# Kernel optimization log

Hardware: AMD Instinct MI355X
Metric: run time of the kernel (lower is better)

The kernel has to match this reference:

```python
import jax, jax.numpy as jnp
import numpy as np

NUM_CLASSES = 151  # Visual Genome object classes
PRED_DIM = 51      # predicate distribution channels (50 predicates + bg)


def _conv2d(x, w, pad):
    # x: [B, Cin, H, W], w: [Cout, Cin, kh, kw]
    return jax.lax.conv_general_dilated(
        x, w, window_strides=(1, 1), padding=[(pad, pad), (pad, pad)],
        dimension_numbers=("NCHW", "OIHW", "NCHW"))


def setup_inputs() -> dict:
    key = jax.random.key(0)
    ks = jax.random.split(key, 12)
    B, N, D = 64, 80, 4096
    K = D // 4  # 1024
    s = 0.02
    return {
        "encoder_reps": jax.random.normal(ks[0], (B, N, D), jnp.float32),
        "obj_preds": jax.random.randint(ks[1], (B, N), 0, NUM_CLASSES, jnp.int32),
        "freq_table": jax.random.normal(ks[2], (NUM_CLASSES * NUM_CLASSES, PRED_DIM), jnp.float32),
        "W_comp": jax.random.normal(ks[3], (D, K), jnp.float32) * s,
        "W_ou1": jax.random.normal(ks[4], (K, K), jnp.float32) * s,
        "W_ofc": jax.random.normal(ks[5], (K, K), jnp.float32) * s,
        "W_decomp": jax.random.normal(ks[6], (K, D), jnp.float32) * s,
        "conv1": jax.random.normal(ks[7], (10, PRED_DIM, 3, 3), jnp.float32) * s,
        "conv2": jax.random.normal(ks[8], (5, 10, 3, 3), jnp.float32) * s,
        "conv3": jax.random.normal(ks[9], (1, 5, 1, 1), jnp.float32) * s,
    }


def reference(encoder_reps, obj_preds, freq_table, W_comp, W_ou1, W_ofc,
              W_decomp, conv1, conv2, conv3):
    B, N, D = encoder_reps.shape
    # obj_comp: Linear(D, D//4, bias=False) + ReLU
    comp = jax.nn.relu(jnp.einsum("bnd,dk->bnk", encoder_reps, W_comp))  # [B,N,K]
    # ou1: Linear(K, K, bias=False) + ReLU
    obj_u1 = jax.nn.relu(jnp.einsum("bnk,kj->bnj", comp, W_ou1))          # [B,N,K]
    # pairwise product indices -> freq_bias.index_with_labels (subj*C + obj)
    pair_idx = obj_preds[:, :, None] * NUM_CLASSES + obj_preds[:, None, :]  # [B,N,N]
    rel_u1 = freq_table[pair_idx]                                          # [B,N,N,51]
    # adjacency via small conv stack + sigmoid
    x = jnp.transpose(rel_u1, (0, 3, 1, 2))      # [B,51,N,N]
    x = _conv2d(x, conv1, pad=1)                 # [B,10,N,N]
    x = _conv2d(x, conv2, pad=1)                 # [B,5,N,N]
    x = _conv2d(x, conv3, pad=0)                 # [B,1,N,N]
    adj = jax.nn.sigmoid(x[:, 0])                # [B,N,N]
    # normalized Laplacian: D^-1/2 (A + I) D^-1/2
    A_hat = adj + jnp.eye(N, dtype=adj.dtype)[None]
    d = (jnp.sum(A_hat, axis=2) + 1e-5) ** (-0.5)                          # [B,N]
    L_hat = d[:, :, None] * A_hat * d[:, None, :]                          # [B,N,N]
    ofl_u = jnp.einsum("bnm,bmk->bnk", L_hat, obj_u1)                      # [B,N,K]
    # ofc_u + obj_decomp + residual
    u_m = jax.nn.relu(jnp.einsum("bnk,kj->bnj", ofl_u, W_ofc))
    decomp = jax.nn.relu(jnp.einsum("bnk,kd->bnd", u_m, W_decomp))
    return decomp + encoder_reps
```

## Files before the change

kernel.cpp:

```cpp
#include <hip/hip_runtime.h>
#include <hip/hip_bf16.h>
#include <math.h>

typedef __bf16 bf16x8 __attribute__((ext_vector_type(8)));
typedef float floatx4 __attribute__((ext_vector_type(4)));
typedef float float4v __attribute__((ext_vector_type(4)));
typedef float float2v __attribute__((ext_vector_type(2)));
typedef unsigned short ushortx4 __attribute__((ext_vector_type(4)));
typedef unsigned short ushortx8 __attribute__((ext_vector_type(8)));

__device__ __forceinline__ unsigned short f2bf(float f) {
    unsigned int u = __builtin_bit_cast(unsigned int, f);
    u += 0x7FFFu + ((u >> 16) & 1u);
    return (unsigned short)(u >> 16);
}
__device__ __forceinline__ float bf2f(unsigned short h) {
    unsigned int u = ((unsigned int)h) << 16;
    return __builtin_bit_cast(float, u);
}

__device__ __forceinline__ void gload_lds16(const void* g, void* l) {
    __builtin_amdgcn_global_load_lds(
        (const __attribute__((address_space(1))) unsigned int*)g,
        (__attribute__((address_space(3))) unsigned int*)l, 16, 0, 0);
}

__global__ __launch_bounds__(256) void cast_bf16_kernel(
    const float* __restrict__ in, unsigned short* __restrict__ out, long n8)
{
    long i = (long)blockIdx.x * 256 + threadIdx.x;
    long stride = (long)gridDim.x * 256;
    for (; i < n8; i += stride) {
        float4v a = reinterpret_cast<const float4v*>(in)[2 * i];
        float4v b = reinterpret_cast<const float4v*>(in)[2 * i + 1];
        ushortx8 h;
        #pragma unroll
        for (int q = 0; q < 4; ++q) { h[q] = f2bf(a[q]); h[4 + q] = f2bf(b[q]); }
        reinterpret_cast<ushortx8*>(out)[i] = h;
    }
}

__global__ __launch_bounds__(256) void reduce_relu_kernel(
    const unsigned short* __restrict__ p, unsigned short* __restrict__ out,
    long n8, long half_elems)
{
    long i = (long)blockIdx.x * 256 + threadIdx.x;
    long stride = (long)gridDim.x * 256;
    const ushortx8* p0 = reinterpret_cast<const ushortx8*>(p);
    const ushortx8* p1 = reinterpret_cast<const ushortx8*>(p + half_elems);
    for (; i < n8; i += stride) {
        ushortx8 a = p0[i], b = p1[i];
        ushortx8 h;
        #pragma unroll
        for (int q = 0; q < 8; ++q)
            h[q] = f2bf(fmaxf(bf2f(a[q]) + bf2f(b[q]), 0.0f));
        reinterpret_cast<ushortx8*>(out)[i] = h;
    }
}

__global__ __launch_bounds__(256) void prep_kernel(
    const float* __restrict__ w1, const float* __restrict__ w2,
    const float* __restrict__ w3, float* __restrict__ W1e,
    float* __restrict__ w23)
{
    for (int idx = threadIdx.x; idx < 4590; idx += 256) {
        int ci = idx / 90, rem = idx % 90;
        int tap = rem / 10, co = rem % 10;
        int di = tap / 3, dj = tap % 3;
        W1e[idx] = w1[((co * 51 + ci) * 3 + di) * 3 + dj];
    }
    if (threadIdx.x < 90) {
        int tap = threadIdx.x / 10, c10 = threadIdx.x % 10;
        int di = tap / 3, dj = tap % 3;
        float s = 0.f;
        #pragma unroll
        for (int c5 = 0; c5 < 5; ++c5)
            s = fmaf(w3[c5], w2[((c5 * 10 + c10) * 3 + di) * 3 + dj], s);
        w23[threadIdx.x] = s;
    }
}

__global__ __launch_bounds__(256) void fp1_kernel(
    const float* __restrict__ freq, const float* __restrict__ W1e,
    float* __restrict__ Fp1)
{
    __shared__ float W1s[4590];
    for (int idx = threadIdx.x; idx < 4590; idx += 256)
        W1s[idx] = W1e[idx];
    __syncthreads();
    int p = blockIdx.x * 256 + threadIdx.x;
    if (p >= 22801) return;
    float2v acc[45];
    #pragma unroll
    for (int t = 0; t < 45; ++t) { acc[t][0] = 0.f; acc[t][1] = 0.f; }
    const float* fr = freq + (size_t)p * 51;
    for (int ci = 0; ci < 51; ++ci) {
        float v = fr[ci];
        const float2v* wrow = reinterpret_cast<const float2v*>(&W1s[ci * 90]);
        #pragma unroll
        for (int t = 0; t < 45; ++t) {
            float2v w = wrow[t];
            acc[t][0] = fmaf(v, w[0], acc[t][0]);
            acc[t][1] = fmaf(v, w[1], acc[t][1]);
        }
    }
    float2v* out = reinterpret_cast<float2v*>(Fp1 + (size_t)p * 90);
    #pragma unroll
    for (int t = 0; t < 45; ++t) out[t] = acc[t];
}

__global__ __launch_bounds__(320) void gather_kernel(
    const int* __restrict__ preds, const float* __restrict__ Fp1,
    float* __restrict__ h1)
{
    __shared__ int pb[80];
    const int b = blockIdx.y;
    const int tid = threadIdx.x;
    if (tid < 80) pb[tid] = preds[b * 80 + tid];
    __syncthreads();
    const int i = blockIdx.x * 4 + tid / 80;
    const int j = tid % 80;
    float2v acc[5];
    #pragma unroll
    for (int q = 0; q < 5; ++q) { acc[q][0] = 0.f; acc[q][1] = 0.f; }
    #pragma unroll
    for (int di = 0; di < 3; ++di) {
        int ii = i + di - 1;
        if (ii < 0 || ii >= 80) continue;
        int pi = pb[ii] * 151;
        #pragma unroll
        for (int dj = 0; dj < 3; ++dj) {
            int jj = j + dj - 1;
            if (jj < 0 || jj >= 80) continue;
            const float2v* row = reinterpret_cast<const float2v*>(
                Fp1 + (size_t)(pi + pb[jj]) * 90 + (di * 3 + dj) * 10);
            #pragma unroll
            for (int q = 0; q < 5; ++q) {
                float2v v = row[q];
                acc[q][0] += v[0];
                acc[q][1] += v[1];
            }
        }
    }
    float2v* out = reinterpret_cast<float2v*>(
        h1 + ((size_t)b * 6400 + i * 80 + j) * 10);
    #pragma unroll
    for (int q = 0; q < 5; ++q) out[q] = acc[q];
}

__global__ __launch_bounds__(320) void conv23_kernel(
    const float* __restrict__ h1, const float* __restrict__ w23g,
    float* __restrict__ adj)
{
    __shared__ float w23s[90];
    const int tid = threadIdx.x;
    if (tid < 90) w23s[tid] = w23g[tid];
    __syncthreads();
    const int b = blockIdx.y;
    const int i = blockIdx.x * 4 + tid / 80;
    const int j = tid % 80;
    float t = 0.f;
    #pragma unroll
    for (int di = 0; di < 3; ++di) {
        int ii = i + di - 1;
        if (ii < 0 || ii >= 80) continue;
        #pragma unroll
        for (int dj = 0; dj < 3; ++dj) {
            int jj = j + dj - 1;
            if (jj < 0 || jj >= 80) continue;
            const float2v* hp = reinterpret_cast<const float2v*>(
                h1 + ((size_t)b * 6400 + ii * 80 + jj) * 10);
            const float* wp = w23s + (di * 3 + dj) * 10;
            #pragma unroll
            for (int q = 0; q < 5; ++q) {
                float2v v = hp[q];
                t = fmaf(v[0], wp[2 * q], t);
                t = fmaf(v[1], wp[2 * q + 1], t);
            }
        }
    }
    adj[(size_t)b * 6400 + i * 80 + j] = 1.0f / (1.0f + __expf(-t));
}

__global__ __launch_bounds__(128) void degree_kernel(
    const float* __restrict__ adj, float* __restrict__ deg)
{
    int b = blockIdx.x;
    int i = threadIdx.x;
    if (i >= 80) return;
    const float* row = adj + (size_t)b * 6400 + i * 80;
    float s = 1.0f + 1e-5f;
    for (int jj = 0; jj < 80; ++jj) s += row[jj];
    deg[b * 80 + i] = rsqrtf(s);
}

__global__ __launch_bounds__(256) void transpose_cast(
    const float* __restrict__ in, unsigned short* __restrict__ out,
    int R, int C)
{
    __shared__ float t[32][33];
    const int tx = threadIdx.x & 31;
    const int ty = threadIdx.x >> 5;
    const int r0 = blockIdx.y * 32, c0 = blockIdx.x * 32;
    #pragma unroll
    for (int k = 0; k < 4; ++k)
        t[ty + k * 8][tx] = in[(size_t)(r0 + ty + k * 8) * C + c0 + tx];
    __syncthreads();
    #pragma unroll
    for (int k = 0; k < 4; ++k)
        out[(size_t)(c0 + ty + k * 8) * R + r0 + tx] = f2bf(t[tx][ty + k * 8]);
}

template<int MODE>
__global__ __launch_bounds__(256) void gemm_pipe(
    const unsigned short* __restrict__ Ap, const unsigned short* __restrict__ Bt,
    void* __restrict__ Cp, const float* __restrict__ Rp,
    int M, int N, int lda, int kh)
{
    __shared__ unsigned short Al[3][128 * 32];
    __shared__ unsigned short Bl[3][128 * 32];

    const int tid  = threadIdx.x;
    const int bm   = blockIdx.x * 128;
    const int bn   = blockIdx.y * 128;
    const int zoff = blockIdx.z * kh;
    const int wave = tid >> 6;
    const int lane = tid & 63;
    const int wm   = (wave >> 1) * 64;
    const int wn   = (wave & 1) * 64;
    const int lr   = lane & 15;
    const int lk   = (lane >> 4) * 8;
    const int lkz  = lk ^ ((lr & 1) << 3) ^ (((lr >> 1) & 1) << 4);

    floatx4 acc[4][4];
    #pragma unroll
    for (int i = 0; i < 4; ++i)
        #pragma unroll
        for (int j = 0; j < 4; ++j)
            #pragma unroll
            for (int r = 0; r < 4; ++r) acc[i][j][r] = 0.0f;

    auto stage = [&](int buf, int k0) {
        #pragma unroll
        for (int it = 0; it < 2; ++it) {
            int idx = tid + it * 256;
            int r = idx >> 2, kc = (idx & 3) * 8;
            int kcz = kc ^ ((r & 1) << 3) ^ (((r >> 1) & 1) << 4);
            gload_lds16(&Ap[(size_t)(bm + r) * lda + k0 + kcz],
                        &Al[buf][idx * 8]);
        }
        #pragma unroll
        for (int it = 0; it < 2; ++it) {
            int idx = tid + it * 256;
            int r = idx >> 2, kc = (idx & 3) * 8;
            int kcz = kc ^ ((r & 1) << 3) ^ (((r >> 1) & 1) << 4);
            gload_lds16(&Bt[(size_t)(bn + r) * lda + k0 + kcz],
                        &Bl[buf][idx * 8]);
        }
    };

    const int nt = kh >> 5;
    stage(0, zoff);
    if (nt > 1) stage(1, zoff + 32);

    for (int t = 0; t < nt; ++t) {
        if (t < nt - 1) {
            asm volatile("s_waitcnt vmcnt(4)" ::: "memory");
        } else {
            asm volatile("s_waitcnt vmcnt(0)" ::: "memory");
        }
        __builtin_amdgcn_s_barrier();
        __builtin_amdgcn_sched_barrier(0);
        if (t + 2 < nt) stage((t + 2) % 3, zoff + ((t + 2) << 5));

        const int cur = t % 3;
        bf16x8 af[4], bfv[4];
        #pragma unroll
        for (int mi = 0; mi < 4; ++mi)
            af[mi] = *reinterpret_cast<const bf16x8*>(
                &Al[cur][(wm + mi * 16 + lr) * 32 + lkz]);
        #pragma unroll
        for (int ni = 0; ni < 4; ++ni)
            bfv[ni] = *reinterpret_cast<const bf16x8*>(
                &Bl[cur][(wn + ni * 16 + lr) * 32 + lkz]);
        #pragma unroll
        for (int mi = 0; mi < 4; ++mi)
            #pragma unroll
            for (int ni = 0; ni < 4; ++ni)
                acc[mi][ni] = __builtin_amdgcn_mfma_f32_16x16x32_bf16(
                    af[mi], bfv[ni], acc[mi][ni], 0, 0, 0);
    }

    #pragma unroll
    for (int mi = 0; mi < 4; ++mi) {
        #pragma unroll
        for (int ni = 0; ni < 4; ++ni) {
            #pragma unroll
            for (int r = 0; r < 4; ++r) {
                int row = bm + wm + mi * 16 + (lane >> 4) * 4 + r;
                int col = bn + wn + ni * 16 + lr;
                size_t off = (size_t)row * N + col;
                if (MODE == 0) {
                    ((unsigned short*)Cp)[off] = f2bf(fmaxf(acc[mi][ni][r], 0.f));
                } else if (MODE == 1) {
                    ((float*)Cp)[off] = fmaxf(acc[mi][ni][r], 0.f) + Rp[off];
                } else {
                    ((unsigned short*)Cp)[(size_t)blockIdx.z * M * N + off] =
                        f2bf(acc[mi][ni][r]);
                }
            }
        }
    }
}

__global__ __launch_bounds__(256) void gemm_f32a(
    const float* __restrict__ Ap, const unsigned short* __restrict__ Bt,
    unsigned short* __restrict__ Cp, int M, int N, int lda)
{
    __shared__ unsigned short Al[2][128 * 40];
    __shared__ unsigned short Bl[2][128 * 32];
    const int tid  = threadIdx.x;
    const int bm   = blockIdx.x * 128;
    const int bn   = blockIdx.y * 128;
    const int wave = tid >> 6;
    const int lane = tid & 63;
    const int wm   = (wave >> 1) * 64;
    const int wn   = (wave & 1) * 64;
    const int lr   = lane & 15;
    const int lk   = (lane >> 4) * 8;

    floatx4 acc[4][4];
    #pragma unroll
    for (int i = 0; i < 4; ++i)
        #pragma unroll
        for (int j = 0; j < 4; ++j)
            #pragma unroll
            for (int r = 0; r < 4; ++r) acc[i][j][r] = 0.0f;

    auto stage = [&](int buf, int k0) {
        #pragma unroll
        for (int it = 0; it < 4; ++it) {
            int idx = tid + it * 256;
            int r = idx >> 3, kc = (idx & 7) * 4;
            float4v v = *reinterpret_cast<const float4v*>(
                &Ap[(size_t)(bm + r) * lda + k0 + kc]);
            ushortx4 h;
            #pragma unroll
            for (int q = 0; q < 4; ++q) h[q] = f2bf(v[q]);
            *reinterpret_cast<ushortx4*>(&Al[buf][r * 40 + kc]) = h;
        }
        #pragma unroll
        for (int it = 0; it < 2; ++it) {
            int idx = tid + it * 256;
            gload_lds16(&Bt[(size_t)(bn + (idx >> 2)) * lda + k0 + (idx & 3) * 8],
                        &Bl[buf][idx * 8]);
        }
    };
    stage(0, 0);
    __syncthreads();
    const int nt = lda >> 5;
    int cur = 0;
    for (int t = 0; t < nt; ++t) {
        if (t + 1 < nt) stage(cur ^ 1, (t + 1) << 5);
        bf16x8 af[4], bfv[4];
        #pragma unroll
        for (int mi = 0; mi < 4; ++mi)
            af[mi] = *reinterpret_cast<const bf16x8*>(
                &Al[cur][(wm + mi * 16 + lr) * 40 + lk]);
        #pragma unroll
        for (int ni = 0; ni < 4; ++ni)
            bfv[ni] = *reinterpret_cast<const bf16x8*>(
                &Bl[cur][(wn + ni * 16 + lr) * 32 + lk]);
        #pragma unroll
        for (int mi = 0; mi < 4; ++mi)
            #pragma unroll
            for (int ni = 0; ni < 4; ++ni)
                acc[mi][ni] = __builtin_amdgcn_mfma_f32_16x16x32_bf16(
                    af[mi], bfv[ni], acc[mi][ni], 0, 0, 0);
        __syncthreads();
        cur ^= 1;
    }
    #pragma unroll
    for (int mi = 0; mi < 4; ++mi)
        #pragma unroll
        for (int ni = 0; ni < 4; ++ni)
            #pragma unroll
            for (int r = 0; r < 4; ++r) {
                int row = bm + wm + mi * 16 + (lane >> 4) * 4 + r;
                int col = bn + wn + ni * 16 + lr;
                Cp[(size_t)row * N + col] = f2bf(fmaxf(acc[mi][ni][r], 0.f));
            }
}

__global__ __launch_bounds__(256) void laplacian_kernel(
    const float* __restrict__ adj, const float* __restrict__ deg,
    const unsigned short* __restrict__ u_in, unsigned short* __restrict__ ofl)
{
    __shared__ float wl[6400];
    __shared__ unsigned short ul[80 * 256];
    const int b   = blockIdx.y;
    const int kq  = blockIdx.x;
    const int tid = threadIdx.x;
    const int ko  = tid & 31;
    const int ngrp = tid >> 5;

    const float* ab = adj + (size_t)b * 6400;
    const float* db = deg + b * 80;
    for (int idx = tid; idx < 6400; idx += 256) {
        int n = idx / 80;
        int m = idx - n * 80;
        float w = ab[idx] + (n == m ? 1.0f : 0.0f);
        wl[idx] = w * db[m];
    }
    const unsigned short* ub = u_in + (size_t)b * 80 * 1024 + kq * 256;
    #pragma unroll
    for (int it = 0; it < 10; ++it) {
        int idx = tid + it * 256;
        int m   = idx >> 5;
        int c8  = (idx & 31) * 8;
        *reinterpret_cast<ushortx8*>(&ul[m * 256 + c8]) =
            *reinterpret_cast<const ushortx8*>(&ub[(size_t)m * 1024 + c8]);
    }
    __syncthreads();

    float acc[10][8];
    #pragma unroll
    for (int ni = 0; ni < 10; ++ni)
        #pragma unroll
        for (int q = 0; q < 8; ++q) acc[ni][q] = 0.0f;

    for (int m = 0; m < 80; ++m) {
        ushortx8 uv = *reinterpret_cast<const ushortx8*>(&ul[m * 256 + ko * 8]);
        float uf[8];
        #pragma unroll
        for (int q = 0; q < 8; ++q) uf[q] = bf2f(uv[q]);
        #pragma unroll
        for (int ni = 0; ni < 10; ++ni) {
            float wv = wl[(ngrp * 10 + ni) * 80 + m];
            #pragma unroll
            for (int q = 0; q < 8; ++q)
                acc[ni][q] = fmaf(wv, uf[q], acc[ni][q]);
        }
    }
    #pragma unroll
    for (int ni = 0; ni < 10; ++ni) {
        int n = ngrp * 10 + ni;
        float dn = db[n];
        ushortx8 o;
        #pragma unroll
        for (int q = 0; q < 8; ++q) o[q] = f2bf(acc[ni][q] * dn);
        *reinterpret_cast<ushortx8*>(
            &ofl[((size_t)(b * 80 + n)) * 1024 + kq * 256 + ko * 8]) = o;
    }
}

extern "C" void kernel_launch(void* const* d_in, const int* in_sizes, int n_in,
                              void* d_out, int out_size, void* d_ws, size_t ws_size,
                              hipStream_t stream)
{
    const float* enc   = (const float*)d_in[0];
    const int*   preds = (const int*)d_in[1];
    const float* freq  = (const float*)d_in[2];
    const float* Wc    = (const float*)d_in[3];
    const float* Wou1  = (const float*)d_in[4];
    const float* Wofc  = (const float*)d_in[5];
    const float* Wdec  = (const float*)d_in[6];
    const float* w1    = (const float*)d_in[7];
    const float* w2    = (const float*)d_in[8];
    const float* w3    = (const float*)d_in[9];

    const int M = 5120;
    unsigned short* comp  = (unsigned short*)d_ws;
    unsigned short* obju  = comp + (size_t)M * 1024;
    unsigned short* r1    = obju + (size_t)M * 1024;
    unsigned short* oflu  = r1;
    float*          h1    = (float*)r1;
    unsigned short* P     = r1;
    unsigned short* r2    = r1 + 8192000;
    unsigned short* um    = r2;
    float*          Fp1   = (float*)r2;
    unsigned short* Wcb   = r2 + (size_t)M * 1024;
    unsigned short* Wou1b = Wcb + (size_t)1024 * 4096;
    unsigned short* Wofcb = Wou1b + (size_t)1024 * 1024;
    unsigned short* Wdecb = Wofcb + (size_t)1024 * 1024;
    float*          W1e   = (float*)(Wdecb + (size_t)4096 * 1024);
    float*          w23   = W1e + 4590;
    float*          adj   = w23 + 90;
    float*          deg   = adj + (size_t)64 * 6400;
    unsigned short* encb  = (unsigned short*)(deg + 5120);
    const size_t need_bytes =
        ((size_t)(encb - comp) + (size_t)M * 4096) * sizeof(unsigned short);
    const bool use_encb = ws_size >= need_bytes;

    prep_kernel<<<1, 256, 0, stream>>>(w1, w2, w3, W1e, w23);
    transpose_cast<<<dim3(32, 128), 256, 0, stream>>>(Wc, Wcb, 4096, 1024);
    transpose_cast<<<dim3(32, 32), 256, 0, stream>>>(Wou1, Wou1b, 1024, 1024);
    transpose_cast<<<dim3(32, 32), 256, 0, stream>>>(Wofc, Wofcb, 1024, 1024);
    transpose_cast<<<dim3(128, 32), 256, 0, stream>>>(Wdec, Wdecb, 1024, 4096);

    fp1_kernel<<<90, 256, 0, stream>>>(freq, W1e, Fp1);
    gather_kernel<<<dim3(20, 64), 320, 0, stream>>>(preds, Fp1, h1);
    conv23_kernel<<<dim3(20, 64), 320, 0, stream>>>(h1, w23, adj);
    degree_kernel<<<64, 128, 0, stream>>>(adj, deg);

    if (use_encb) {
        cast_bf16_kernel<<<2048, 256, 0, stream>>>(
            enc, encb, (long)M * 4096 / 8);
        gemm_pipe<2><<<dim3(40, 8, 2), 256, 0, stream>>>(
            encb, Wcb, P, nullptr, M, 1024, 4096, 2048);
        reduce_relu_kernel<<<2048, 256, 0, stream>>>(
            P, comp, (long)M * 1024 / 8, (size_t)M * 1024);
    } else {
        gemm_f32a<<<dim3(40, 8), 256, 0, stream>>>(
            enc, Wcb, comp, M, 1024, 4096);
    }
    gemm_pipe<0><<<dim3(40, 8), 256, 0, stream>>>(
        comp, Wou1b, obju, nullptr, M, 1024, 1024, 1024);
    laplacian_kernel<<<dim3(4, 64), 256, 0, stream>>>(adj, deg, obju, oflu);
    gemm_pipe<0><<<dim3(40, 8), 256, 0, stream>>>(
        oflu, Wofcb, um, nullptr, M, 1024, 1024, 1024);
    gemm_pipe<1><<<dim3(40, 32), 256, 0, stream>>>(
        um, Wdecb, d_out, enc, M, 4096, 1024, 1024);
}
```

Measured before the change: 349.2 us.

## Use 256x256 8-wave GEMM tiles with 3-way split-K for square GEMMs

Replaces the 128x128 four-wave GEMM with a 512-thread 256x256 tile kernel (gemm8). It double-buffers 64-wide K steps, interleaves LDS reads, prefetch and MFMA, and raises wave priority around the MFMA blocks. The three 1024-wide GEMMs now use 3-way split-K with bf16 partials and a three-input reduce kernel to fill the machine despite only 80 output tiles. The cost is extra partial-sum traffic and bf16 rounding of partials. The 4096-output GEMM uses the big tile directly. A simpler fallback kernel covers the small-workspace path.

After: 331.9 us. -5.0%, faster.

```diff
diff --git a/kernel.cpp b/kernel.cpp
--- a/kernel.cpp
+++ b/kernel.cpp
@@ -40,20 +40,22 @@
     }
 }
 
-__global__ __launch_bounds__(256) void reduce_relu_kernel(
-    const unsigned short* __restrict__ p, unsigned short* __restrict__ out,
-    long n8, long half_elems)
+__global__ __launch_bounds__(256) void reduce3_kernel(
+    const unsigned short* __restrict__ p0, const unsigned short* __restrict__ p1,
+    const unsigned short* __restrict__ p2, unsigned short* __restrict__ out,
+    long n8)
 {
     long i = (long)blockIdx.x * 256 + threadIdx.x;
     long stride = (long)gridDim.x * 256;
-    const ushortx8* p0 = reinterpret_cast<const ushortx8*>(p);
-    const ushortx8* p1 = reinterpret_cast<const ushortx8*>(p + half_elems);
+    const ushortx8* a0 = reinterpret_cast<const ushortx8*>(p0);
+    const ushortx8* a1 = reinterpret_cast<const ushortx8*>(p1);
+    const ushortx8* a2 = reinterpret_cast<const ushortx8*>(p2);
     for (; i < n8; i += stride) {
-        ushortx8 a = p0[i], b = p1[i];
+        ushortx8 x = a0[i], y = a1[i], zv = a2[i];
         ushortx8 h;
         #pragma unroll
         for (int q = 0; q < 8; ++q)
-            h[q] = f2bf(fmaxf(bf2f(a[q]) + bf2f(b[q]), 0.0f));
+            h[q] = f2bf(fmaxf(bf2f(x[q]) + bf2f(y[q]) + bf2f(zv[q]), 0.0f));
         reinterpret_cast<ushortx8*>(out)[i] = h;
     }
 }
@@ -212,26 +214,178 @@
 }
 
 template<int MODE>
-__global__ __launch_bounds__(256) void gemm_pipe(
+__global__ __launch_bounds__(512, 1) void gemm8(
     const unsigned short* __restrict__ Ap, const unsigned short* __restrict__ Bt,
     void* __restrict__ Cp, const float* __restrict__ Rp,
-    int M, int N, int lda, int kh)
-{
-    __shared__ unsigned short Al[3][128 * 32];
-    __shared__ unsigned short Bl[3][128 * 32];
-
+    unsigned short* __restrict__ P1, unsigned short* __restrict__ P2,
+    int M, int N, int lda, int khA, int khB)
+{
+    __shared__ __align__(16) unsigned short Al[2][2][8192];
+    __shared__ __align__(16) unsigned short Bl[2][2][8192];
+
+    const int tid = threadIdx.x;
+    const int bm  = blockIdx.x * 256;
+    const int bn  = blockIdx.y * 256;
+    const int z   = blockIdx.z;
+    const int k0  = z ? (khA + (z - 1) * khB) : 0;
+    const int kh  = z ? khB : khA;
+    const int nt  = kh >> 6;
+
+    const int w    = tid >> 6;
+    const int lane = tid & 63;
+    const int wr   = w >> 2;
+    const int wc   = w & 3;
+    const int lr   = lane & 15;
+    const int lo   = lane >> 4;
+    const int r3   = lr & 3;
+    const int soct = (lo ^ r3) * 8;
+
+    floatx4 acc[8][4];
+    #pragma unroll
+    for (int i = 0; i < 8; ++i)
+        #pragma unroll
+        for (int j = 0; j < 4; ++j)
+            #pragma unroll
+            for (int r = 0; r < 4; ++r) acc[i][j][r] = 0.0f;
+
+    auto stageA = [&](int buf, int ks, int kt) {
+        #pragma unroll
+        for (int it = 0; it < 2; ++it) {
+            int d = tid + it * 512;
+            int row = d >> 2, s = d & 3;
+            gload_lds16(
+                &Ap[(size_t)(bm + row) * lda + kt + ks * 32 + ((s ^ (row & 3)) * 8)],
+                &Al[buf][ks][d * 8]);
+        }
+    };
+    auto stageB = [&](int buf, int ks, int kt) {
+        #pragma unroll
+        for (int it = 0; it < 2; ++it) {
+            int d = tid + it * 512;
+            int row = d >> 2, s = d & 3;
+            gload_lds16(
+                &Bt[(size_t)(bn + row) * lda + kt + ks * 32 + ((s ^ (row & 3)) * 8)],
+                &Bl[buf][ks][d * 8]);
+        }
+    };
+
+    stageA(0, 0, k0); stageB(0, 0, k0); stageA(0, 1, k0); stageB(0, 1, k0);
+
+    for (int t = 0; t < nt; ++t) {
+        const int cur = t & 1;
+        const int nxt = cur ^ 1;
+        const int ktn = k0 + ((t + 1) << 6);
+        const bool pf = (t + 1 < nt);
+
+        asm volatile("s_waitcnt vmcnt(4)" ::: "memory");
+        __builtin_amdgcn_s_barrier();
+        __builtin_amdgcn_sched_barrier(0);
+        bf16x8 b0[4], af[4];
+        #pragma unroll
+        for (int n = 0; n < 4; ++n)
+            b0[n] = *reinterpret_cast<const bf16x8*>(
+                &Bl[cur][0][(wc * 64 + n * 16 + lr) * 32 + soct]);
+        #pragma unroll
+        for (int m = 0; m < 4; ++m)
+            af[m] = *reinterpret_cast<const bf16x8*>(
+                &Al[cur][0][(wr * 128 + m * 16 + lr) * 32 + soct]);
+        if (pf) stageA(nxt, 0, ktn);
+        __builtin_amdgcn_s_setprio(1);
+        #pragma unroll
+        for (int m = 0; m < 4; ++m)
+            #pragma unroll
+            for (int n = 0; n < 4; ++n)
+                acc[m][n] = __builtin_amdgcn_mfma_f32_16x16x32_bf16(
+                    af[m], b0[n], acc[m][n], 0, 0, 0);
+        __builtin_amdgcn_s_setprio(0);
+
+        #pragma unroll
+        for (int m = 0; m < 4; ++m)
+            af[m] = *reinterpret_cast<const bf16x8*>(
+                &Al[cur][0][(wr * 128 + (m + 4) * 16 + lr) * 32 + soct]);
+        if (pf) stageB(nxt, 0, ktn);
+        __builtin_amdgcn_s_setprio(1);
+        #pragma unroll
+        for (int m = 0; m < 4; ++m)
+            #pragma unroll
+            for (int n = 0; n < 4; ++n)
+                acc[m + 4][n] = __builtin_amdgcn_mfma_f32_16x16x32_bf16(
+                    af[m], b0[n], acc[m + 4][n], 0, 0, 0);
+        __builtin_amdgcn_s_setprio(0);
+
+        if (pf) { asm volatile("s_waitcnt vmcnt(4)" ::: "memory"); }
+        else    { asm volatile("s_waitcnt vmcnt(0)" ::: "memory"); }
+        __builtin_amdgcn_s_barrier();
+        __builtin_amdgcn_sched_barrier(0);
+        #pragma unroll
+        for (int n = 0; n < 4; ++n)
+            b0[n] = *reinterpret_cast<const bf16x8*>(
+                &Bl[cur][1][(wc * 64 + n * 16 + lr) * 32 + soct]);
+        #pragma unroll
+        for (int m = 0; m < 4; ++m)
+            af[m] = *reinterpret_cast<const bf16x8*>(
+                &Al[cur][1][(wr * 128 + m * 16 + lr) * 32 + soct]);
+        if (pf) stageA(nxt, 1, ktn);
+        __builtin_amdgcn_s_setprio(1);
+        #pragma unroll
+        for (int m = 0; m < 4; ++m)
+            #pragma unroll
+            for (int n = 0; n < 4; ++n)
+                acc[m][n] = __builtin_amdgcn_mfma_f32_16x16x32_bf16(
+                    af[m], b0[n], acc[m][n], 0, 0, 0);
+        __builtin_amdgcn_s_setprio(0);
+
+        #pragma unroll
+        for (int m = 0; m < 4; ++m)
+            af[m] = *reinterpret_cast<const bf16x8*>(
+                &Al[cur][1][(wr * 128 + (m + 4) * 16 + lr) * 32 + soct]);
+        if (pf) stageB(nxt, 1, ktn);
+        __builtin_amdgcn_s_setprio(1);
+        #pragma unroll
+        for (int m = 0; m < 4; ++m)
+            #pragma unroll
+            for (int n = 0; n < 4; ++n)
+                acc[m + 4][n] = __builtin_amdgcn_mfma_f32_16x16x32_bf16(
+                    af[m], b0[n], acc[m + 4][n], 0, 0, 0);
+        __builtin_amdgcn_s_setprio(0);
+    }
+
+    unsigned short* dstp = (MODE == 2)
+        ? ((z == 0) ? (unsigned short*)Cp : ((z == 1) ? P1 : P2)) : nullptr;
+    #pragma unroll
+    for (int mi = 0; mi < 8; ++mi) {
+        #pragma unroll
+        for (int ni = 0; ni < 4; ++ni) {
+            #pragma unroll
+            for (int rr = 0; rr < 4; ++rr) {
+                int row = bm + wr * 128 + mi * 16 + lo * 4 + rr;
+                int col = bn + wc * 64 + ni * 16 + lr;
+                size_t off = (size_t)row * N + col;
+                if (MODE == 1) {
+                    ((float*)Cp)[off] = fmaxf(acc[mi][ni][rr], 0.f) + Rp[off];
+                } else {
+                    dstp[off] = f2bf(acc[mi][ni][rr]);
+                }
+            }
+        }
+    }
+}
+
+__global__ __launch_bounds__(256) void gemm_pipe0(
+    const unsigned short* __restrict__ Ap, const unsigned short* __restrict__ Bt,
+    unsigned short* __restrict__ Cp, int M, int N, int lda)
+{
+    __shared__ unsigned short Al[2][128 * 32];
+    __shared__ unsigned short Bl[2][128 * 32];
     const int tid  = threadIdx.x;
     const int bm   = blockIdx.x * 128;
     const int bn   = blockIdx.y * 128;
-    const int zoff = blockIdx.z * kh;
     const int wave = tid >> 6;
     const int lane = tid & 63;
     const int wm   = (wave >> 1) * 64;
     const int wn   = (wave & 1) * 64;
     const int lr   = lane & 15;
     const int lk   = (lane >> 4) * 8;
-    const int lkz  = lk ^ ((lr & 1) << 3) ^ (((lr >> 1) & 1) << 4);
-
     floatx4 acc[4][4];
     #pragma unroll
     for (int i = 0; i < 4; ++i)
@@ -239,78 +393,54 @@
         for (int j = 0; j < 4; ++j)
             #pragma unroll
             for (int r = 0; r < 4; ++r) acc[i][j][r] = 0.0f;
-
-    auto stage = [&](int buf, int k0) {
+    auto stage = [&](int buf, int kq) {
         #pragma unroll
         for (int it = 0; it < 2; ++it) {
             int idx = tid + it * 256;
-            int r = idx >> 2, kc = (idx & 3) * 8;
-            int kcz = kc ^ ((r & 1) << 3) ^ (((r >> 1) & 1) << 4);
-            gload_lds16(&Ap[(size_t)(bm + r) * lda + k0 + kcz],
+            gload_lds16(&Ap[(size_t)(bm + (idx >> 2)) * lda + kq + (idx & 3) * 8],
                         &Al[buf][idx * 8]);
         }
         #pragma unroll
         for (int it = 0; it < 2; ++it) {
             int idx = tid + it * 256;
-            int r = idx >> 2, kc = (idx & 3) * 8;
-            int kcz = kc ^ ((r & 1) << 3) ^ (((r >> 1) & 1) << 4);
-            gload_lds16(&Bt[(size_t)(bn + r) * lda + k0 + kcz],
+            gload_lds16(&Bt[(size_t)(bn + (idx >> 2)) * lda + kq + (idx & 3) * 8],
                         &Bl[buf][idx * 8]);
         }
     };
-
-    const int nt = kh >> 5;
-    stage(0, zoff);
-    if (nt > 1) stage(1, zoff + 32);
-
+    stage(0, 0);
+    __syncthreads();
+    const int nt = lda >> 5;
+    int cur = 0;
     for (int t = 0; t < nt; ++t) {
-        if (t < nt - 1) {
-            asm volatile("s_waitcnt vmcnt(4)" ::: "memory");
-        } else {
-            asm volatile("s_waitcnt vmcnt(0)" ::: "memory");
-        }
-        __builtin_amdgcn_s_barrier();
-        __builtin_amdgcn_sched_barrier(0);
-        if (t + 2 < nt) stage((t + 2) % 3, zoff + ((t + 2) << 5));
-
-        const int cur = t % 3;
+        if (t + 1 < nt) stage(cur ^ 1, (t + 1) << 5);
         bf16x8 af[4], bfv[4];
         #pragma unroll
         for (int mi = 0; mi < 4; ++mi)
             af[mi] = *reinterpret_cast<const bf16x8*>(
-                &Al[cur][(wm + mi * 16 + lr) * 32 + lkz]);
+                &Al[cur][(wm + mi * 16 + lr) * 32 + lk]);
         #pragma unroll
         for (int ni = 0; ni < 4; ++ni)
             bfv[ni] = *reinterpret_cast<const bf16x8*>(
-                &Bl[cur][(wn + ni * 16 + lr) * 32 + lkz]);
+                &Bl[cur][(wn + ni * 16 + lr) * 32 + lk]);
         #pragma unroll
         for (int mi = 0; mi < 4; ++mi)
             #pragma unroll
             for (int ni = 0; ni < 4; ++ni)
                 acc[mi][ni] = __builtin_amdgcn_mfma_f32_16x16x32_bf16(
                     af[mi], bfv[ni], acc[mi][ni], 0, 0, 0);
-    }
-
-    #pragma unroll
-    for (int mi = 0; mi < 4; ++mi) {
-        #pragma unroll
-        for (int ni = 0; ni < 4; ++ni) {
+        __syncthreads();
+        cur ^= 1;
+    }
+    #pragma unroll
+    for (int mi = 0; mi < 4; ++mi)
+        #pragma unroll
+        for (int ni = 0; ni < 4; ++ni)
             #pragma unroll
             for (int r = 0; r < 4; ++r) {
                 int row = bm + wm + mi * 16 + (lane >> 4) * 4 + r;
                 int col = bn + wn + ni * 16 + lr;
-                size_t off = (size_t)row * N + col;
-                if (MODE == 0) {
-                    ((unsigned short*)Cp)[off] = f2bf(fmaxf(acc[mi][ni][r], 0.f));
-                } else if (MODE == 1) {
-                    ((float*)Cp)[off] = fmaxf(acc[mi][ni][r], 0.f) + Rp[off];
-                } else {
-                    ((unsigned short*)Cp)[(size_t)blockIdx.z * M * N + off] =
-                        f2bf(acc[mi][ni][r]);
-                }
+                Cp[(size_t)row * N + col] = f2bf(fmaxf(acc[mi][ni][r], 0.f));
             }
-        }
-    }
 }
 
 __global__ __launch_bounds__(256) void gemm_f32a(
@@ -328,7 +458,6 @@
     const int wn   = (wave & 1) * 64;
     const int lr   = lane & 15;
     const int lk   = (lane >> 4) * 8;
-
     floatx4 acc[4][4];
     #pragma unroll
     for (int i = 0; i < 4; ++i)
@@ -336,7 +465,6 @@
         for (int j = 0; j < 4; ++j)
             #pragma unroll
             for (int r = 0; r < 4; ++r) acc[i][j][r] = 0.0f;
-
     auto stage = [&](int buf, int k0) {
         #pragma unroll
         for (int it = 0; it < 4; ++it) {
@@ -470,16 +598,16 @@
     const float* w3    = (const float*)d_in[9];
 
     const int M = 5120;
+    const size_t SLAB = (size_t)M * 1024;
     unsigned short* comp  = (unsigned short*)d_ws;
-    unsigned short* obju  = comp + (size_t)M * 1024;
-    unsigned short* r1    = obju + (size_t)M * 1024;
+    unsigned short* obju  = comp + SLAB;
+    unsigned short* r1    = obju + SLAB;
     unsigned short* oflu  = r1;
     float*          h1    = (float*)r1;
-    unsigned short* P     = r1;
     unsigned short* r2    = r1 + 8192000;
     unsigned short* um    = r2;
     float*          Fp1   = (float*)r2;
-    unsigned short* Wcb   = r2 + (size_t)M * 1024;
+    unsigned short* Wcb   = r2 + SLAB;
     unsigned short* Wou1b = Wcb + (size_t)1024 * 4096;
     unsigned short* Wofcb = Wou1b + (size_t)1024 * 1024;
     unsigned short* Wdecb = Wofcb + (size_t)1024 * 1024;
@@ -491,6 +619,9 @@
     const size_t need_bytes =
         ((size_t)(encb - comp) + (size_t)M * 4096) * sizeof(unsigned short);
     const bool use_encb = ws_size >= need_bytes;
+    unsigned short* Q0 = encb;
+    unsigned short* Q1 = encb + SLAB;
+    unsigned short* Q2 = encb + 2 * SLAB;
 
     prep_kernel<<<1, 256, 0, stream>>>(w1, w2, w3, W1e, w23);
     transpose_cast<<<dim3(32, 128), 256, 0, stream>>>(Wc, Wcb, 4096, 1024);
@@ -504,21 +635,25 @@
     degree_kernel<<<64, 128, 0, stream>>>(adj, deg);
 
     if (use_encb) {
-        cast_bf16_kernel<<<2048, 256, 0, stream>>>(
-            enc, encb, (long)M * 4096 / 8);
-        gemm_pipe<2><<<dim3(40, 8, 2), 256, 0, stream>>>(
-            encb, Wcb, P, nullptr, M, 1024, 4096, 2048);
-        reduce_relu_kernel<<<2048, 256, 0, stream>>>(
-            P, comp, (long)M * 1024 / 8, (size_t)M * 1024);
+        cast_bf16_kernel<<<2048, 256, 0, stream>>>(enc, encb, (long)M * 4096 / 8);
+        gemm8<2><<<dim3(20, 4, 3), 512, 0, stream>>>(
+            encb, Wcb, r1, nullptr, r2, obju, M, 1024, 4096, 1408, 1344);
+        reduce3_kernel<<<2048, 256, 0, stream>>>(r1, r2, obju, comp, SLAB / 8);
+        gemm8<2><<<dim3(20, 4, 3), 512, 0, stream>>>(
+            comp, Wou1b, Q0, nullptr, Q1, Q2, M, 1024, 1024, 384, 320);
+        reduce3_kernel<<<2048, 256, 0, stream>>>(Q0, Q1, Q2, obju, SLAB / 8);
     } else {
-        gemm_f32a<<<dim3(40, 8), 256, 0, stream>>>(
-            enc, Wcb, comp, M, 1024, 4096);
-    }
-    gemm_pipe<0><<<dim3(40, 8), 256, 0, stream>>>(
-        comp, Wou1b, obju, nullptr, M, 1024, 1024, 1024);
+        gemm_f32a<<<dim3(40, 8), 256, 0, stream>>>(enc, Wcb, comp, M, 1024, 4096);
+        gemm_pipe0<<<dim3(40, 8), 256, 0, stream>>>(comp, Wou1b, obju, M, 1024, 1024);
+    }
     laplacian_kernel<<<dim3(4, 64), 256, 0, stream>>>(adj, deg, obju, oflu);
-    gemm_pipe<0><<<dim3(40, 8), 256, 0, stream>>>(
-        oflu, Wofcb, um, nullptr, M, 1024, 1024, 1024);
-    gemm_pipe<1><<<dim3(40, 32), 256, 0, stream>>>(
-        um, Wdecb, d_out, enc, M, 4096, 1024, 1024);
-}
+    if (use_encb) {
+        gemm8<2><<<dim3(20, 4, 3), 512, 0, stream>>>(
+            oflu, Wofcb, Q0, nullptr, Q1, Q2, M, 1024, 1024, 384, 320);
+        reduce3_kernel<<<2048, 256, 0, stream>>>(Q0, Q1, Q2, um, SLAB / 8);
+    } else {
+        gemm_pipe0<<<dim3(40, 8), 256, 0, stream>>>(oflu, Wofcb, um, M, 1024, 1024);
+    }
+    gemm8<1><<<dim3(20, 16, 1), 512, 0, stream>>>(
+        um, Wdecb, d_out, enc, nullptr, nullptr, M, 4096, 1024, 1024, 0);
+}
```
